# Performance work log

Hardware: AMD Instinct MI355X
Metric: run time of the kernel (lower is better)

The kernel has to match this reference:

```python
import jax, jax.numpy as jnp
import numpy as np

B, D_CAT, C_IN, C_OUT, K, H, W = 16, 512, 256, 256, 3, 64, 64


def setup_inputs() -> dict:
    key = jax.random.key(0)
    ks = jax.random.split(key, 9)
    inp = {
        "x": jax.random.normal(ks[0], (B, C_IN, H, W), dtype=jnp.float32),
        "y": jax.random.normal(ks[1], (B, D_CAT), dtype=jnp.float32),
        # EqualLinear stack: d_catin -> in_channels, then n_dl=2 layers in_channels -> in_channels
        "w0": jax.random.normal(ks[2], (C_IN, D_CAT), dtype=jnp.float32) / np.sqrt(D_CAT),
        "b0": jnp.zeros((C_IN,), dtype=jnp.float32),
        "w1": jax.random.normal(ks[3], (C_IN, C_IN), dtype=jnp.float32) / np.sqrt(C_IN),
        "b1": jnp.zeros((C_IN,), dtype=jnp.float32),
        "w2": jax.random.normal(ks[4], (C_IN, C_IN), dtype=jnp.float32) / np.sqrt(C_IN),
        "b2": jnp.zeros((C_IN,), dtype=jnp.float32),
        # shared conv weight (O, I, k, k), modulated per sample
        "conv_w": jax.random.normal(ks[5], (C_OUT, C_IN, K, K), dtype=jnp.float32) / np.sqrt(C_IN * K * K),
    }
    return inp


def _lrelu(z):
    # nn.LeakyReLU default negative_slope = 0.01
    return jnp.where(z >= 0, z, 0.01 * z)


def reference(x, y, w0, b0, w1, b1, w2, b2, conv_w):
    # style MLP (EqualLinear stack with LeakyReLU)
    s = _lrelu(y @ w0.T + b0)          # (B, C_in)
    s = _lrelu(s @ w1.T + b1)
    s = _lrelu(s @ w2.T + b2)
    # Per-sample weight modulation: conv(x[b], W * s[b, None, :, None, None]).
    # Since the scale is per input channel (no demodulation), this is exactly
    # equivalent to scaling the input channels and running one shared conv —
    # the fused form a custom kernel would use.
    x_mod = x * s[:, :, None, None]    # (B, C_in, H, W)
    out = jax.lax.conv_general_dilated(
        x_mod, conv_w,
        window_strides=(1, 1),
        padding=((1, 1), (1, 1)),
        dimension_numbers=("NCHW", "OIHW", "NCHW"),
    )  # (B, C_out, H, W); conv has bias=False in _DyConv
    return out
```

## Files before the change

kernel.cpp:

```cpp
#include <hip/hip_runtime.h>

typedef short bf16x8 __attribute__((ext_vector_type(8)));
typedef float f32x4 __attribute__((ext_vector_type(4)));
typedef unsigned short ushort8 __attribute__((ext_vector_type(8)));
typedef unsigned short ushort4v __attribute__((ext_vector_type(4)));

#define BATCH 16
#define DCAT 512
#define CIN 256
#define COUT 256
#define HH 64
#define WW 64
#define HP 66
#define WP 66
#define PLANE (HP * WP * 8)
#define AHALO 52224
#define BBUF 32768

__device__ __forceinline__ unsigned short f2bf(float f) {
  unsigned int u = __float_as_uint(f);
  unsigned int r = (u + 0x7fffu + ((u >> 16) & 1u)) >> 16;
  return (unsigned short)r;
}

template <int IN_DIM>
__global__ void __launch_bounds__(256) mlp_layer(const float* __restrict__ in,
                                                 const float* __restrict__ w,
                                                 const float* __restrict__ bias,
                                                 float* __restrict__ out) {
  int wid = threadIdx.x >> 6, lane = threadIdx.x & 63;
  int oidx = blockIdx.x * 4 + wid;
  int b = oidx >> 8, c = oidx & 255;
  const float* wr = w + (size_t)c * IN_DIM;
  const float* ir = in + (size_t)b * IN_DIM;
  float sum = 0.f;
#pragma unroll
  for (int d0 = 0; d0 < IN_DIM; d0 += 256) {
    f32x4 wv = *(const f32x4*)(wr + d0 + lane * 4);
    f32x4 iv = *(const f32x4*)(ir + d0 + lane * 4);
    sum += wv[0] * iv[0] + wv[1] * iv[1] + wv[2] * iv[2] + wv[3] * iv[3];
  }
#pragma unroll
  for (int off = 32; off; off >>= 1) sum += __shfl_xor(sum, off, 64);
  if (lane == 0) {
    float a = sum + bias[c];
    out[oidx] = a >= 0.f ? a : 0.01f * a;
  }
}

__global__ void __launch_bounds__(256) prep_all(const float* __restrict__ t1,
                                                const float* __restrict__ w2,
                                                const float* __restrict__ b2,
                                                const float* __restrict__ x,
                                                const float* __restrict__ cw,
                                                unsigned short* __restrict__ xpad,
                                                unsigned short* __restrict__ wt) {
  int blk = blockIdx.x;
  int tid = threadIdx.x;

  if (blk >= 1024) {
    int idx = (blk - 1024) * 256 + tid;
    int t = idx / 16384;
    int r = idx - t * 16384;
    int o = r >> 6, i4 = r & 63;
    ushort4v v;
#pragma unroll
    for (int j = 0; j < 4; j++) v[j] = f2bf(cw[(o * 256 + i4 * 4 + j) * 9 + t]);
    *(ushort4v*)(wt + ((size_t)(t * COUT + o)) * CIN + i4 * 4) = v;
    return;
  }

  int h = blk & 1, c8 = (blk >> 1) & 31, b = blk >> 6;
  int wid = tid >> 6, lane = tid & 63;

  float tv = t1[b * CIN + tid];
  float pj[8];
#pragma unroll
  for (int j = 0; j < 8; j++) pj[j] = w2[(size_t)(c8 * 8 + j) * CIN + tid] * tv;

  const float* xb = x + ((size_t)(b * CIN + c8 * 8)) * (HH * WW);
  int gg0 = h * 512 + tid;
  int gg1 = gg0 + 256;
  int hh0 = (gg0 >> 4) + 1, w00 = (gg0 & 15) * 4 + 1;
  int hh1 = (gg1 >> 4) + 1, w01 = (gg1 & 15) * 4 + 1;
  int base0 = (hh0 - 1) * WW + (w00 - 1);
  int base1 = (hh1 - 1) * WW + (w01 - 1);
  f32x4 v0[8], v1[8];
#pragma unroll
  for (int j = 0; j < 8; j++) v0[j] = *(const f32x4*)(xb + j * (HH * WW) + base0);
#pragma unroll
  for (int j = 0; j < 8; j++) v1[j] = *(const f32x4*)(xb + j * (HH * WW) + base1);

#pragma unroll
  for (int off = 32; off; off >>= 1)
#pragma unroll
    for (int j = 0; j < 8; j++) pj[j] += __shfl_xor(pj[j], off, 64);
  __shared__ float red[4][8];
  __shared__ float sv_sh[8];
  if (lane == 0)
#pragma unroll
    for (int j = 0; j < 8; j++) red[wid][j] = pj[j];
  __syncthreads();
  if (tid < 8) {
    float a = red[0][tid] + red[1][tid] + red[2][tid] + red[3][tid] + b2[c8 * 8 + tid];
    sv_sh[tid] = a >= 0.f ? a : 0.01f * a;
  }
  __syncthreads();
  float sv[8];
#pragma unroll
  for (int j = 0; j < 8; j++) sv[j] = sv_sh[j];

  unsigned short* xp = xpad + ((size_t)(b * 32 + c8)) * PLANE;

  if (tid < 130) {
    int i = h * 130 + tid;
    int bh, bw;
    if (i < 66) { bh = 0; bw = i; }
    else if (i < 132) { bh = 65; bw = i - 66; }
    else if (i < 196) { bh = i - 132 + 1; bw = 0; }
    else { bh = i - 196 + 1; bw = 65; }
    ushort8 z = {0, 0, 0, 0, 0, 0, 0, 0};
    *(ushort8*)(xp + (bh * WP + bw) * 8) = z;
  }

  unsigned short* op0 = xp + (hh0 * WP + w00) * 8;
  unsigned short* op1 = xp + (hh1 * WP + w01) * 8;
#pragma unroll
  for (int t2 = 0; t2 < 4; t2++) {
    ushort8 o;
#pragma unroll
    for (int j = 0; j < 8; j++) o[j] = f2bf(v0[j][t2] * sv[j]);
    *(ushort8*)(op0 + t2 * 8) = o;
  }
#pragma unroll
  for (int t2 = 0; t2 < 4; t2++) {
    ushort8 o;
#pragma unroll
    for (int j = 0; j < 8; j++) o[j] = f2bf(v1[j][t2] * sv[j]);
    *(ushort8*)(op1 + t2 * 8) = o;
  }
}

__device__ __forceinline__ void gl2lds16(const void* g, void* l) {
  __builtin_amdgcn_global_load_lds((const __attribute__((address_space(1))) void*)g,
                                   (__attribute__((address_space(3))) void*)l, 16, 0, 0);
}

#define WAIT_LGKM0()                                        \
  asm volatile("s_waitcnt lgkmcnt(0)" ::: "memory");        \
  __builtin_amdgcn_sched_barrier(0)

__global__ void __launch_bounds__(512, 1) gemm_conv(const unsigned short* __restrict__ xpad,
                                                    const unsigned short* __restrict__ wt,
                                                    float* __restrict__ out) {
  __shared__ __align__(16) char lds[AHALO + 2 * BBUF];
  int tid = threadIdx.x;
  int wid = tid >> 6, lane = tid & 63;
  int bid = blockIdx.x;
  int m_t = (bid & 7) * 32 + (bid >> 3);
  int m0 = m_t << 8;
  int b = m0 >> 12;
  int h0 = (m0 >> 6) & 63;
  int wm = wid & 1, wn = wid >> 1;

  f32x4 acc[8][4];
#pragma unroll
  for (int mi = 0; mi < 8; mi++)
#pragma unroll
    for (int ni = 0; ni < 4; ni++) acc[mi][ni] = (f32x4){0.f, 0.f, 0.f, 0.f};

  const unsigned short* aSrc[7];
#pragma unroll
  for (int i = 0; i < 7; i++) {
    int c = (i * 8 + wid) * 64 + lane;
    int e = c >> 3, cs = c & 7;
    int gs = cs ^ (e & 7);
    int rh = e / 68, wc = e - rh * 68;
    aSrc[i] = xpad + ((size_t)((b * 32 + gs) * HP + (h0 + rh))) * (WP * 8) + wc * 8;
  }

  int o_l = tid >> 3;
  int csb = tid & 7;
  const unsigned short* bL = wt + o_l * CIN + ((csb ^ (o_l & 7)) * 8);

  int qa = lane >> 4;
  int l15 = lane & 15;
  int rB = wn * 64 + l15;
  int offB0 = rB * 128 + ((qa ^ (rB & 7)) * 16);
  int offB1 = rB * 128 + (((qa + 4) ^ (rB & 7)) * 16);

#define STAGE_B4(BUF, BG)                                               \
  do {                                                                  \
    char* dB_ = lds + AHALO + (BUF) * BBUF + wid * 1024;                \
    const unsigned short* bg_ = (BG);                                   \
    _Pragma("unroll")                                                   \
    for (int q = 0; q < 4; q++) gl2lds16(bg_ + q * 64 * CIN, dB_ + q * 8192); \
  } while (0)

#define STAGE_A(KOFS)                                                   \
  do {                                                                  \
    size_t ko_ = (KOFS);                                                \
    _Pragma("unroll")                                                   \
    for (int i = 0; i < 6; i++)                                         \
      gl2lds16(aSrc[i] + ko_, lds + (i * 8 + wid) * 1024);              \
    if (wid < 3) gl2lds16(aSrc[6] + ko_, lds + (48 + wid) * 1024);      \
  } while (0)

  STAGE_A(0);
  STAGE_B4(0, bL);
  asm volatile("s_waitcnt vmcnt(0)" ::: "memory");
  __builtin_amdgcn_s_barrier();

  int cur = 0;
  for (int kc2 = 0; kc2 < 4; kc2++) {
    for (int kh = 0; kh < 3; kh++) {
      for (int kw = 0; kw < 3; kw++) {
        int tap = kh * 3 + kw;

        int eb = (wm * 2 + kh) * 68 + l15 + kw;
        int s0 = eb & 7, s1 = (eb + 4) & 7;
        int a00 = eb * 128 + ((qa ^ s0) * 16);
        int a01 = (eb + 68) * 128 + ((qa ^ s1) * 16);
        int a10 = eb * 128 + (((qa + 4) ^ s0) * 16);
        int a11 = (eb + 68) * 128 + (((qa + 4) ^ s1) * 16);
        const char* Bb = lds + AHALO + cur * BBUF;

        if (tap < 8) {
          STAGE_B4(cur ^ 1, bL + (size_t)(tap + 1) * (COUT * CIN) + kc2 * 64);
        } else if (kc2 < 3) {
          STAGE_B4(cur ^ 1, bL + (kc2 + 1) * 64);
        }
        {
          bf16x8 av[8], bv[4];
#pragma unroll
          for (int mi = 0; mi < 4; mi++) {
            av[mi] = *(const bf16x8*)(lds + a00 + mi * 2048);
            av[4 + mi] = *(const bf16x8*)(lds + a01 + mi * 2048);
          }
#pragma unroll
          for (int ni = 0; ni < 4; ni++)
            bv[ni] = *(const bf16x8*)(Bb + offB0 + ni * 2048);
          asm volatile("s_waitcnt vmcnt(4)" ::: "memory");
          __builtin_amdgcn_s_barrier();
          WAIT_LGKM0();
          __builtin_amdgcn_s_setprio(1);
#pragma unroll
          for (int mi = 0; mi < 8; mi++)
#pragma unroll
            for (int ni = 0; ni < 4; ni++)
              acc[mi][ni] = __builtin_amdgcn_mfma_f32_16x16x32_bf16(av[mi], bv[ni],
                                                                    acc[mi][ni], 0, 0, 0);
          __builtin_amdgcn_s_setprio(0);
          __builtin_amdgcn_s_barrier();
        }

        {
          bf16x8 aw[8], bw[4];
#pragma unroll
          for (int mi = 0; mi < 4; mi++) {
            aw[mi] = *(const bf16x8*)(lds + a10 + mi * 2048);
            aw[4 + mi] = *(const bf16x8*)(lds + a11 + mi * 2048);
          }
#pragma unroll
          for (int ni = 0; ni < 4; ni++)
            bw[ni] = *(const bf16x8*)(Bb + offB1 + ni * 2048);
          __builtin_amdgcn_s_barrier();
          WAIT_LGKM0();
          __builtin_amdgcn_s_setprio(1);
#pragma unroll
          for (int mi = 0; mi < 8; mi++)
#pragma unroll
            for (int ni = 0; ni < 4; ni++)
              acc[mi][ni] = __builtin_amdgcn_mfma_f32_16x16x32_bf16(aw[mi], bw[ni],
                                                                    acc[mi][ni], 0, 0, 0);
          __builtin_amdgcn_s_setprio(0);
          __builtin_amdgcn_s_barrier();
        }

        cur ^= 1;
      }
    }
    if (kc2 < 3) {
      STAGE_A((size_t)(kc2 + 1) * 8 * PLANE);
      asm volatile("s_waitcnt vmcnt(0)" ::: "memory");
      __builtin_amdgcn_s_barrier();
    }
  }

  int pixbase = m0 & 4095;
  int quad = lane >> 4;
  int col = lane & 15;
#pragma unroll
  for (int mi = 0; mi < 8; mi++) {
    int pm = pixbase + wm * 128 + mi * 16 + quad * 4;
#pragma unroll
    for (int ni = 0; ni < 4; ni++) {
      int on = wn * 64 + ni * 16 + col;
      float* op = out + ((size_t)(b * COUT + on) << 12) + pm;
      *(f32x4*)op = acc[mi][ni];
    }
  }
}

extern "C" void kernel_launch(void* const* d_in, const int* in_sizes, int n_in,
                              void* d_out, int out_size, void* d_ws, size_t ws_size,
                              hipStream_t stream) {
  const float* x = (const float*)d_in[0];
  const float* y = (const float*)d_in[1];
  const float* w0 = (const float*)d_in[2];
  const float* b0 = (const float*)d_in[3];
  const float* w1 = (const float*)d_in[4];
  const float* b1 = (const float*)d_in[5];
  const float* w2 = (const float*)d_in[6];
  const float* b2 = (const float*)d_in[7];
  const float* cw = (const float*)d_in[8];
  float* out = (float*)d_out;

  char* ws = (char*)d_ws;
  unsigned short* xpad = (unsigned short*)ws;
  unsigned short* wt = (unsigned short*)(ws + 35684352);
  float* t0 = (float*)(ws + 35684352 + 2359296);
  float* t1 = (float*)(ws + 35684352 + 2359296 + 16384);

  mlp_layer<DCAT><<<BATCH * CIN / 4, 256, 0, stream>>>(y, w0, b0, t0);
  mlp_layer<CIN><<<BATCH * CIN / 4, 256, 0, stream>>>(t0, w1, b1, t1);
  prep_all<<<1024 + 576, 256, 0, stream>>>(t1, w2, b2, x, cw, xpad, wt);
  gemm_conv<<<BATCH * HH * WW / 256, 512, 0, stream>>>(xpad, wt, out);
}
```

Baseline: 228.3 us.

## Triple-buffer weight tiles and split MFMA work into four interleaved clusters

Moves the B (weight) staging from double to triple buffering with a prefetch distance of two taps, which raises LDS use to AHALO plus three B buffers. Each tap's 64 MFMAs are split into four 16-MFMA clusters, and one global-to-LDS load is issued before each cluster, so loads and compute are interleaved at finer grain. The A-halo restage moves inside the tap loop at the end of each K-chunk. The aim is to hide global load latency and spread register pressure more evenly. The cost is twice as many barriers per tap and more LDS, which could limit overlap.

New measurement: 215.0 us. 5.8% less time.

```diff
diff --git a/kernel.cpp b/kernel.cpp
--- a/kernel.cpp
+++ b/kernel.cpp
@@ -153,7 +153,7 @@
 __global__ void __launch_bounds__(512, 1) gemm_conv(const unsigned short* __restrict__ xpad,
                                                     const unsigned short* __restrict__ wt,
                                                     float* __restrict__ out) {
-  __shared__ __align__(16) char lds[AHALO + 2 * BBUF];
+  __shared__ __align__(16) char lds[AHALO + 3 * BBUF];
   int tid = threadIdx.x;
   int wid = tid >> 6, lane = tid & 63;
   int bid = blockIdx.x;
@@ -189,14 +189,6 @@
   int offB0 = rB * 128 + ((qa ^ (rB & 7)) * 16);
   int offB1 = rB * 128 + (((qa + 4) ^ (rB & 7)) * 16);
 
-#define STAGE_B4(BUF, BG)                                               \
-  do {                                                                  \
-    char* dB_ = lds + AHALO + (BUF) * BBUF + wid * 1024;                \
-    const unsigned short* bg_ = (BG);                                   \
-    _Pragma("unroll")                                                   \
-    for (int q = 0; q < 4; q++) gl2lds16(bg_ + q * 64 * CIN, dB_ + q * 8192); \
-  } while (0)
-
 #define STAGE_A(KOFS)                                                   \
   do {                                                                  \
     size_t ko_ = (KOFS);                                                \
@@ -206,16 +198,42 @@
     if (wid < 3) gl2lds16(aSrc[6] + ko_, lds + (48 + wid) * 1024);      \
   } while (0)
 
+#define CLUSTER16(MB, AV, BV)                                               \
+  do {                                                                      \
+    __builtin_amdgcn_s_setprio(1);                                          \
+    _Pragma("unroll")                                                       \
+    for (int mi = 0; mi < 4; mi++)                                          \
+      _Pragma("unroll")                                                     \
+      for (int ni = 0; ni < 4; ni++)                                        \
+        acc[(MB) + mi][ni] = __builtin_amdgcn_mfma_f32_16x16x32_bf16(       \
+            AV[mi], BV[ni], acc[(MB) + mi][ni], 0, 0, 0);                   \
+    __builtin_amdgcn_s_setprio(0);                                          \
+  } while (0)
+
   STAGE_A(0);
-  STAGE_B4(0, bL);
+  {
+    char* d0 = lds + AHALO + wid * 1024;
+    char* d1 = lds + AHALO + BBUF + wid * 1024;
+    const unsigned short* s1 = bL + (size_t)1 * (COUT * CIN);
+#pragma unroll
+    for (int q = 0; q < 4; q++) gl2lds16(bL + q * 64 * CIN, d0 + q * 8192);
+#pragma unroll
+    for (int q = 0; q < 4; q++) gl2lds16(s1 + q * 64 * CIN, d1 + q * 8192);
+  }
   asm volatile("s_waitcnt vmcnt(0)" ::: "memory");
   __builtin_amdgcn_s_barrier();
 
-  int cur = 0;
   for (int kc2 = 0; kc2 < 4; kc2++) {
     for (int kh = 0; kh < 3; kh++) {
       for (int kw = 0; kw < 3; kw++) {
         int tap = kh * 3 + kw;
+        int T = kc2 * 9 + tap;
+        const char* Bb = lds + AHALO + (T % 3) * BBUF;
+        int T2 = T + 2;
+        bool st = T2 < 36;
+        const unsigned short* sB =
+            bL + (size_t)(T2 % 9) * (COUT * CIN) + (T2 / 9) * 64;
+        char* dB = lds + AHALO + (T2 % 3) * BBUF + wid * 1024;
 
         int eb = (wm * 2 + kh) * 68 + l15 + kw;
         int s0 = eb & 7, s1 = (eb + 4) & 7;
@@ -223,67 +241,62 @@
         int a01 = (eb + 68) * 128 + ((qa ^ s1) * 16);
         int a10 = eb * 128 + (((qa + 4) ^ s0) * 16);
         int a11 = (eb + 68) * 128 + (((qa + 4) ^ s1) * 16);
-        const char* Bb = lds + AHALO + cur * BBUF;
-
-        if (tap < 8) {
-          STAGE_B4(cur ^ 1, bL + (size_t)(tap + 1) * (COUT * CIN) + kc2 * 64);
-        } else if (kc2 < 3) {
-          STAGE_B4(cur ^ 1, bL + (kc2 + 1) * 64);
+
+        bf16x8 va[4], vb[4], b0v[4], b1v[4];
+
+#pragma unroll
+        for (int mi = 0; mi < 4; mi++)
+          va[mi] = *(const bf16x8*)(lds + a00 + mi * 2048);
+#pragma unroll
+        for (int ni = 0; ni < 4; ni++)
+          b0v[ni] = *(const bf16x8*)(Bb + offB0 + ni * 2048);
+        if (st) gl2lds16(sB, dB);
+        __builtin_amdgcn_s_barrier();
+        WAIT_LGKM0();
+        CLUSTER16(0, va, b0v);
+        __builtin_amdgcn_s_barrier();
+
+#pragma unroll
+        for (int mi = 0; mi < 4; mi++)
+          vb[mi] = *(const bf16x8*)(lds + a01 + mi * 2048);
+        if (st) gl2lds16(sB + 64 * CIN, dB + 8192);
+        __builtin_amdgcn_s_barrier();
+        WAIT_LGKM0();
+        CLUSTER16(4, vb, b0v);
+        __builtin_amdgcn_s_barrier();
+
+#pragma unroll
+        for (int mi = 0; mi < 4; mi++)
+          va[mi] = *(const bf16x8*)(lds + a10 + mi * 2048);
+#pragma unroll
+        for (int ni = 0; ni < 4; ni++)
+          b1v[ni] = *(const bf16x8*)(Bb + offB1 + ni * 2048);
+        if (st) gl2lds16(sB + 128 * CIN, dB + 16384);
+        __builtin_amdgcn_s_barrier();
+        WAIT_LGKM0();
+        CLUSTER16(0, va, b1v);
+        __builtin_amdgcn_s_barrier();
+
+#pragma unroll
+        for (int mi = 0; mi < 4; mi++)
+          vb[mi] = *(const bf16x8*)(lds + a11 + mi * 2048);
+        if (st) {
+          gl2lds16(sB + 192 * CIN, dB + 24576);
+          asm volatile("s_waitcnt vmcnt(4)" ::: "memory");
+        } else {
+          asm volatile("s_waitcnt vmcnt(0)" ::: "memory");
         }
-        {
-          bf16x8 av[8], bv[4];
-#pragma unroll
-          for (int mi = 0; mi < 4; mi++) {
-            av[mi] = *(const bf16x8*)(lds + a00 + mi * 2048);
-            av[4 + mi] = *(const bf16x8*)(lds + a01 + mi * 2048);
-          }
-#pragma unroll
-          for (int ni = 0; ni < 4; ni++)
-            bv[ni] = *(const bf16x8*)(Bb + offB0 + ni * 2048);
-          asm volatile("s_waitcnt vmcnt(4)" ::: "memory");
-          __builtin_amdgcn_s_barrier();
-          WAIT_LGKM0();
-          __builtin_amdgcn_s_setprio(1);
-#pragma unroll
-          for (int mi = 0; mi < 8; mi++)
-#pragma unroll
-            for (int ni = 0; ni < 4; ni++)
-              acc[mi][ni] = __builtin_amdgcn_mfma_f32_16x16x32_bf16(av[mi], bv[ni],
-                                                                    acc[mi][ni], 0, 0, 0);
-          __builtin_amdgcn_s_setprio(0);
+        __builtin_amdgcn_s_barrier();
+        WAIT_LGKM0();
+        CLUSTER16(4, vb, b1v);
+        __builtin_amdgcn_s_barrier();
+
+        if (tap == 8 && kc2 < 3) {
+          STAGE_A((size_t)(kc2 + 1) * 8 * PLANE);
+          asm volatile("s_waitcnt vmcnt(0)" ::: "memory");
           __builtin_amdgcn_s_barrier();
         }
-
-        {
-          bf16x8 aw[8], bw[4];
-#pragma unroll
-          for (int mi = 0; mi < 4; mi++) {
-            aw[mi] = *(const bf16x8*)(lds + a10 + mi * 2048);
-            aw[4 + mi] = *(const bf16x8*)(lds + a11 + mi * 2048);
-          }
-#pragma unroll
-          for (int ni = 0; ni < 4; ni++)
-            bw[ni] = *(const bf16x8*)(Bb + offB1 + ni * 2048);
-          __builtin_amdgcn_s_barrier();
-          WAIT_LGKM0();
-          __builtin_amdgcn_s_setprio(1);
-#pragma unroll
-          for (int mi = 0; mi < 8; mi++)
-#pragma unroll
-            for (int ni = 0; ni < 4; ni++)
-              acc[mi][ni] = __builtin_amdgcn_mfma_f32_16x16x32_bf16(aw[mi], bw[ni],
-                                                                    acc[mi][ni], 0, 0, 0);
-          __builtin_amdgcn_s_setprio(0);
-          __builtin_amdgcn_s_barrier();
-        }
-
-        cur ^= 1;
       }
-    }
-    if (kc2 < 3) {
-      STAGE_A((size_t)(kc2 + 1) * 8 * PLANE);
-      asm volatile("s_waitcnt vmcnt(0)" ::: "memory");
-      __builtin_amdgcn_s_barrier();
     }
   }
 
```
